# Optimization experiments

Measured on AMD Instinct MI355X. Metric: run time of the kernel, lower is better.

## Reference

```python
import jax, jax.numpy as jnp
import numpy as np

B, K, N, D = 64, 64, 32768, 2048   # batch, knn neighbors, memory size, feat dim (hardcoded 2048 in source)
NC, NHID, TOPK = 2048, 512, 5      # num clusters, gcn hidden, topk in affinity masking


def setup_inputs() -> dict:
    key = jax.random.key(0)
    ks = jax.random.split(key, 8)
    features = jax.random.normal(ks[0], (N, D), jnp.float32)
    labels = jax.random.randint(ks[1], (N,), 0, NC)
    indexes = jax.random.randint(ks[2], (B,), 0, N)
    ori_knn_neighbor = jax.random.randint(ks[3], (B, K), 0, N)
    s = 0.02
    conv_w = jax.random.normal(ks[4], (2 * D, NHID), jnp.float32) * s
    conv_b = jnp.zeros((NHID,), jnp.float32)
    w1 = jax.random.normal(ks[5], (NHID, NHID), jnp.float32) * s
    b1 = jnp.zeros((NHID,), jnp.float32)
    prelu_a = jnp.full((NHID,), 0.25, jnp.float32)
    w2 = jax.random.normal(ks[6], (NHID, 2), jnp.float32) * s
    b2 = jnp.zeros((2,), jnp.float32)
    return dict(indexes=indexes, features=features, labels=labels,
                ori_knn_neighbor=ori_knn_neighbor, conv_w=conv_w, conv_b=conv_b,
                w1=w1, b1=b1, prelu_a=prelu_a, w2=w2, b2=b2)


def _build_graphs(indexes, features, labels, ori_knn_neighbor):
    # cluster mean features (index_add_ + count normalize), done under no_grad in torch
    counts = jax.ops.segment_sum(jnp.ones((N,), jnp.float32), labels, num_segments=NC)
    clu_sum = jax.ops.segment_sum(features, labels, num_segments=NC)
    clu_mean = clu_sum / jnp.maximum(counts, 1.0)[:, None]

    def per_sample(idx, nbr):
        clu_lab = labels[nbr]                                  # [K]
        cf = clu_mean[clu_lab].at[0].set(features[idx])        # [K, D]
        A = (cf @ cf.T) / 5.0                                  # [K, K]
        j = jnp.arange(K)
        # keep only first occurrence of each cluster label (np.unique return_index)
        dup = jnp.any((clu_lab[:, None] == clu_lab[None, :]) & (j[None, :] < j[:, None]), axis=1)
        keep = (~dup).astype(A.dtype)                          # [K]
        _, ti = jax.lax.top_k(A, TOPK)                         # [K, TOPK]
        m = jnp.zeros_like(A).at[j[:, None], ti].set(1.0)
        m = ((m > 0) & (m.T > 0)).astype(A.dtype) * keep[:, None] * keep[None, :]
        A = A * m
        cf = cf / jnp.linalg.norm(cf, axis=1, keepdims=True)   # row-normalize
        cf = cf - cf[0]                                        # center on query (row 0 -> 0)
        return cf, A

    x, adj = jax.vmap(per_sample)(indexes, ori_knn_neighbor)   # [B,K,D], [B,K,K]
    return jax.lax.stop_gradient(x), jax.lax.stop_gradient(adj)


def reference(indexes, features, labels, ori_knn_neighbor,
              conv_w, conv_b, w1, b1, prelu_a, w2, b2):
    x, adj = _build_graphs(indexes, features, labels, ori_knn_neighbor)
    # GraphConv with MeanAggregator: agg = A @ x, concat, linear, relu
    agg = jnp.einsum('bij,bjd->bid', adj, x)                   # [B,K,D]
    h = jax.nn.relu(jnp.concatenate([x, agg], axis=-1) @ conv_w + conv_b)  # [B,K,NHID]
    h0 = h.reshape(-1, NHID)
    h1 = h0 @ w1 + b1
    h1 = jnp.where(h1 > 0, h1, prelu_a * h1)                   # PReLU(nhid)
    logits = h1 @ w2 + b2                                      # [B*K, 2]
    return jax.nn.softmax(logits.reshape(B, K, 2), axis=2)
```

## Files before the change

kernel.cpp:

```cpp
#include <hip/hip_runtime.h>
#include <hip/hip_bf16.h>

#define BB 64
#define KN 64
#define NPTS 32768
#define DD 2048
#define NCC 2048
#define NH 512
#define MM 4096
#define K2 4096

typedef unsigned short u16;
typedef unsigned int u32;
typedef __attribute__((ext_vector_type(8))) short short8;
typedef __attribute__((ext_vector_type(4))) float f32x4;

__device__ __forceinline__ float bf2f(u32 u){
  union { u32 i; float f; } v; v.i = u << 16; return v.f;
}
__device__ __forceinline__ u16 f2bf(float f){
  union { float f; u32 i; } v; v.f = f;
  u32 x = v.i;
  return (u16)((x + 0x7fffu + ((x >> 16) & 1u)) >> 16);
}

typedef __attribute__((address_space(3))) u32 as3_u32;
typedef const __attribute__((address_space(1))) u32 as1_u32;
__device__ __forceinline__ void glds16(const void* g, void* l){
  __builtin_amdgcn_global_load_lds((as1_u32*)g, (as3_u32*)l, 16, 0, 0);
}

__global__ __launch_bounds__(256) void k_prep(
    const int* __restrict__ labels, int* __restrict__ counts,
    const int* __restrict__ knn, int* __restrict__ used,
    const void* __restrict__ conv_w, u16* __restrict__ cwT, int fcw,
    const void* __restrict__ w1, u16* __restrict__ w1T, int fw1){
  __shared__ u16 tile[64][65];
  int bb = blockIdx.x, t = threadIdx.x;
  if(bb < 128){
    int n = bb*256 + t;
    atomicAdd(&counts[labels[n]], 1);
    return;
  }
  if(bb == 704){
    #pragma unroll
    for(int i=0;i<16;i++){
      int idx = i*256 + t;
      used[labels[knn[idx]]] = 1;
    }
    return;
  }
  const void* src; u16* dst; int Kd, Nd, isf32, tb;
  if(bb < 640){ src=conv_w; dst=cwT; Kd=K2; Nd=NH; isf32=fcw; tb=bb-128; }
  else        { src=w1;     dst=w1T; Kd=NH; Nd=NH; isf32=fw1; tb=bb-640; }
  int nbt = Nd >> 6;
  int k0 = (tb / nbt) << 6;
  int n0 = (tb % nbt) << 6;
  if(isf32){
    const float* s = (const float*)src;
    #pragma unroll
    for(int ph=0; ph<16; ph++){
      int idx = ph*256 + t;
      int r = idx >> 6, c = idx & 63;
      tile[r][c] = f2bf(s[(size_t)(k0+r)*Nd + n0 + c]);
    }
  } else {
    const u16* s = (const u16*)src;
    #pragma unroll
    for(int ph=0; ph<16; ph++){
      int idx = ph*256 + t;
      int r = idx >> 6, c = idx & 63;
      tile[r][c] = s[(size_t)(k0+r)*Nd + n0 + c];
    }
  }
  __syncthreads();
  #pragma unroll
  for(int ph=0; ph<16; ph++){
    int idx = ph*256 + t;
    int r = idx >> 6, c = idx & 63;
    dst[(size_t)(n0+r)*Kd + k0 + c] = tile[c][r];
  }
}

__global__ void k_scan(const int* __restrict__ counts, int* __restrict__ offsets){
  __shared__ int sb[256];
  int t = threadIdx.x;
  int c[8]; int s = 0;
  #pragma unroll
  for(int i=0;i<8;i++){ c[i] = counts[t*8+i]; s += c[i]; }
  sb[t] = s; __syncthreads();
  int v = s;
  for(int off=1; off<256; off<<=1){
    int u = (t>=off) ? sb[t-off] : 0;
    __syncthreads();
    v += u; sb[t] = v;
    __syncthreads();
  }
  int run = v - s;
  #pragma unroll
  for(int i=0;i<8;i++){ offsets[t*8+i] = run; run += c[i]; }
}

__global__ void k_scatter(const int* __restrict__ labels, const int* __restrict__ offsets,
                          int* __restrict__ cursor, int* __restrict__ sorted){
  int n = blockIdx.x*256 + threadIdx.x;
  int c = labels[n];
  int p = atomicAdd(&cursor[c], 1);
  sorted[offsets[c] + p] = n;
}

__global__ __launch_bounds__(256) void k_clumean(
    const void* __restrict__ feat, const int* __restrict__ counts,
    const int* __restrict__ offsets, const int* __restrict__ sorted,
    const int* __restrict__ used, int isf32, float* __restrict__ clu){
  int c = blockIdx.x, t = threadIdx.x;
  if(!used[c]) return;
  __shared__ int ridx[64];
  int cnt = counts[c], start = offsets[c];
  float acc[8] = {0,0,0,0,0,0,0,0};
  for(int base=0; base<cnt; base+=64){
    int take = min(64, cnt-base);
    __syncthreads();
    if(t < take) ridx[t] = sorted[start+base+t];
    __syncthreads();
    if(isf32){
      const float* ff = (const float*)feat;
      int r = 0;
      for(; r+2<=take; r+=2){
        const float* p0 = ff + (size_t)ridx[r]*DD + t*8;
        const float* p1 = ff + (size_t)ridx[r+1]*DD + t*8;
        float4 a0=*(const float4*)p0, b0=*(const float4*)(p0+4);
        float4 a1=*(const float4*)p1, b1=*(const float4*)(p1+4);
        acc[0]+=a0.x+a1.x; acc[1]+=a0.y+a1.y; acc[2]+=a0.z+a1.z; acc[3]+=a0.w+a1.w;
        acc[4]+=b0.x+b1.x; acc[5]+=b0.y+b1.y; acc[6]+=b0.z+b1.z; acc[7]+=b0.w+b1.w;
      }
      if(r < take){
        const float* p0 = ff + (size_t)ridx[r]*DD + t*8;
        float4 a0=*(const float4*)p0, b0=*(const float4*)(p0+4);
        acc[0]+=a0.x; acc[1]+=a0.y; acc[2]+=a0.z; acc[3]+=a0.w;
        acc[4]+=b0.x; acc[5]+=b0.y; acc[6]+=b0.z; acc[7]+=b0.w;
      }
    } else {
      const u16* fb = (const u16*)feat;
      int r = 0;
      for(; r+2<=take; r+=2){
        const u16* p0 = fb + (size_t)ridx[r]*DD + t*8;
        const u16* p1 = fb + (size_t)ridx[r+1]*DD + t*8;
        uint4 v0 = *(const uint4*)p0, v1 = *(const uint4*)p1;
        acc[0]+=bf2f(v0.x&0xffffu)+bf2f(v1.x&0xffffu); acc[1]+=bf2f(v0.x>>16)+bf2f(v1.x>>16);
        acc[2]+=bf2f(v0.y&0xffffu)+bf2f(v1.y&0xffffu); acc[3]+=bf2f(v0.y>>16)+bf2f(v1.y>>16);
        acc[4]+=bf2f(v0.z&0xffffu)+bf2f(v1.z&0xffffu); acc[5]+=bf2f(v0.z>>16)+bf2f(v1.z>>16);
        acc[6]+=bf2f(v0.w&0xffffu)+bf2f(v1.w&0xffffu); acc[7]+=bf2f(v0.w>>16)+bf2f(v1.w>>16);
      }
      if(r < take){
        const u16* p0 = fb + (size_t)ridx[r]*DD + t*8;
        uint4 v0 = *(const uint4*)p0;
        acc[0]+=bf2f(v0.x&0xffffu); acc[1]+=bf2f(v0.x>>16);
        acc[2]+=bf2f(v0.y&0xffffu); acc[3]+=bf2f(v0.y>>16);
        acc[4]+=bf2f(v0.z&0xffffu); acc[5]+=bf2f(v0.z>>16);
        acc[6]+=bf2f(v0.w&0xffffu); acc[7]+=bf2f(v0.w>>16);
      }
    }
  }
  float div = fmaxf((float)cnt, 1.0f);
  float* o = clu + (size_t)c*DD + t*8;
  float4 o0 = make_float4(acc[0]/div, acc[1]/div, acc[2]/div, acc[3]/div);
  float4 o1 = make_float4(acc[4]/div, acc[5]/div, acc[6]/div, acc[7]/div);
  *(float4*)o = o0;
  *(float4*)(o+4) = o1;
}

__global__ __launch_bounds__(256) void k_Apart(
    const void* __restrict__ feat, const float* __restrict__ clu,
    const int* __restrict__ indexes, const int* __restrict__ labels,
    const int* __restrict__ knn, int isf32, float* __restrict__ Apart){
  int b = blockIdx.x >> 2, g = blockIdx.x & 3;
  int t = threadIdx.x;
  __shared__ float cfT[64][68];
  __shared__ int sl[64];
  if(t < 64) sl[t] = labels[knn[b*64 + t]];
  int qidx = indexes[b];
  __syncthreads();

  int i0 = (t & 15)*4, j0 = (t >> 4)*4;
  float acc[4][4];
  #pragma unroll
  for(int a=0;a<4;a++)
    #pragma unroll
    for(int c2=0;c2<4;c2++) acc[a][c2] = 0.f;

  for(int ch=g*8; ch<g*8+8; ch++){
    int dbase = ch*64;
    #pragma unroll
    for(int ps=0; ps<16; ps++){
      int idx = ps*256 + t;
      int k = idx >> 6, dd = idx & 63;
      float v;
      if(k == 0){
        size_t fi = (size_t)qidx*DD + dbase + dd;
        v = isf32 ? ((const float*)feat)[fi] : bf2f(((const u16*)feat)[fi]);
      } else {
        v = clu[(size_t)sl[k]*DD + dbase + dd];
      }
      cfT[dd][k] = v;
    }
    __syncthreads();
    #pragma unroll 4
    for(int dd=0; dd<64; dd++){
      float4 av = *(const float4*)&cfT[dd][i0];
      float4 bv = *(const float4*)&cfT[dd][j0];
      float aa[4] = {av.x, av.y, av.z, av.w};
      float bbv[4] = {bv.x, bv.y, bv.z, bv.w};
      #pragma unroll
      for(int ii=0;ii<4;ii++)
        #pragma unroll
        for(int jj=0;jj<4;jj++)
          acc[ii][jj] += aa[ii]*bbv[jj];
    }
    __syncthreads();
  }

  float* op = Apart + ((size_t)(g*64 + b))*4096;
  #pragma unroll
  for(int ii=0;ii<4;ii++)
    *(float4*)&op[(i0+ii)*64 + j0] = make_float4(acc[ii][0], acc[ii][1], acc[ii][2], acc[ii][3]);
}

__global__ __launch_bounds__(256) void k_Afinal(
    const float* __restrict__ Apart, const int* __restrict__ labels,
    const int* __restrict__ knn,
    float* __restrict__ adj, float* __restrict__ norms){
  int b = blockIdx.x, t = threadIdx.x;
  __shared__ float A[64][65];
  __shared__ unsigned long long mb[64];
  __shared__ int sl[64];
  __shared__ int sk[64];
  if(t < 64) sl[t] = labels[knn[b*64 + t]];
  const float* P = Apart + (size_t)b*4096;
  const size_t gs = (size_t)64*4096;
  #pragma unroll
  for(int ps=0; ps<16; ps++){
    int idx = ps*256 + t;
    float s = P[idx] + P[idx+gs] + P[idx+2*gs] + P[idx+3*gs];
    A[idx>>6][idx&63] = s * 0.2f;
  }
  __syncthreads();
  if(t < 64){
    int dup = 0;
    for(int j=0;j<t;j++) dup |= (sl[j]==sl[t]);
    sk[t] = dup ? 0 : 1;
    unsigned long long chosen = 0;
    const float* row = A[t];
    #pragma unroll
    for(int p=0;p<5;p++){
      float best = -INFINITY; int bi = 0;
      for(int j=0;j<64;j++){
        bool taken = (chosen >> j) & 1ull;
        float v = row[j];
        if(!taken && v > best){ best = v; bi = j; }
      }
      chosen |= (1ull << bi);
    }
    mb[t] = chosen;
    norms[b*64+t] = sqrtf(fmaxf(A[t][t]*5.0f, 0.0f));
  }
  __syncthreads();
  float* O = adj + (size_t)b*4096;
  #pragma unroll
  for(int ps=0; ps<16; ps++){
    int idx = ps*256 + t;
    int i = idx >> 6, j = idx & 63;
    bool on = ((mb[i]>>j)&1ull) && ((mb[j]>>i)&1ull) && sk[i] && sk[j];
    O[idx] = on ? A[i][j] : 0.0f;
  }
}

__global__ __launch_bounds__(256) void k_xagg(
    const void* __restrict__ feat, const float* __restrict__ clu,
    const int* __restrict__ indexes, const int* __restrict__ labels,
    const int* __restrict__ knn, const float* __restrict__ norms,
    const float* __restrict__ adj, int isf32, u16* __restrict__ xab){
  int b = blockIdx.x >> 2, g = blockIdx.x & 3;
  int t = threadIdx.x;
  __shared__ u16  xs[64][512];
  __shared__ float adjs[64][65];
  __shared__ float nzv[64][8];
  __shared__ u16   nzj[64][8];
  __shared__ int   nzc[64];
  __shared__ int   sl[64];
  __shared__ float sn[64];

  const float* Ab = adj + (size_t)b*4096;
  #pragma unroll
  for(int ps=0; ps<16; ps++){
    int idx = ps*256 + t;
    adjs[idx>>6][idx&63] = Ab[idx];
  }
  if(t < 64){
    sl[t] = labels[knn[b*64 + t]];
    sn[t] = 1.0f / fmaxf(norms[b*64 + t], 1e-30f);
  }
  int qidx = indexes[b];
  int d = g*512 + t*2;
  float q0, q1;
  if(isf32){
    float2 qv = *(const float2*)((const float*)feat + (size_t)qidx*DD + d);
    q0 = qv.x; q1 = qv.y;
  } else {
    u32 w = *(const u32*)((const u16*)feat + (size_t)qidx*DD + d);
    q0 = bf2f(w & 0xffffu); q1 = bf2f(w >> 16);
  }
  __syncthreads();
  if(t < 64){
    int c = 0;
    for(int j=0;j<64;j++){
      float v = adjs[t][j];
      if(v != 0.0f && c < 8){ nzv[t][c] = v; nzj[t][c] = (u16)j; c++; }
    }
    nzc[t] = c;
  }
  float inv0 = sn[0];
  q0 *= inv0; q1 *= inv0;

  *(u32*)&xs[0][t*2] = 0u;
  *(u32*)(xab + (size_t)(b*64)*K2 + d) = 0u;
  for(int k=1;k<64;k++){
    float2 cv = *(const float2*)(clu + (size_t)sl[k]*DD + d);
    float invk = sn[k];
    u16 x0 = f2bf(cv.x*invk - q0), x1 = f2bf(cv.y*invk - q1);
    u32 w = (u32)x0 | ((u32)x1 << 16);
    *(u32*)&xs[k][t*2] = w;
    *(u32*)(xab + (size_t)(b*64+k)*K2 + d) = w;
  }
  __syncthreads();

  for(int r=0;r<64;r++){
    float a0 = 0.f, a1 = 0.f;
    int c = nzc[r];
    for(int p=0;p<c;p++){
      float s = nzv[r][p]; int j = nzj[r][p];
      u32 w = *(const u32*)&xs[j][t*2];
      a0 += s*bf2f(w & 0xffffu);
      a1 += s*bf2f(w >> 16);
    }
    u32 w = (u32)f2bf(a0) | ((u32)f2bf(a1) << 16);
    *(u32*)(xab + (size_t)(b*64+r)*K2 + DD + d) = w;
  }
}

template<int EPI>
__global__ __launch_bounds__(256, 2) void k_gemm(
    const u16* __restrict__ Am, const u16* __restrict__ Bt,
    const void* __restrict__ bias, const void* __restrict__ pa,
    int fbias, int fpa,
    void* __restrict__ Cout, int Md, int Nd, int Kd)
{
  __shared__ u16 As[2][64*64];
  __shared__ u16 Bs[2][64*64];
  int t = threadIdx.x;
  int nblk = gridDim.x;
  int bid = (blockIdx.x & 7)*(nblk >> 3) + (blockIdx.x >> 3);
  int nb = Nd >> 6;
  int m0 = (bid / nb) << 6;
  int n0 = (bid % nb) << 6;
  int wave = t >> 6, lane = t & 63;
  int wm = wave >> 1, wn = wave & 1;
  int lm = lane & 15, lq = lane >> 4;
  int lrow = lane >> 3, lcol = lane & 7;

  f32x4 acc[2][2];
  #pragma unroll
  for(int i=0;i<2;i++)
    #pragma unroll
    for(int j=0;j<2;j++) acc[i][j] = (f32x4){0.f,0.f,0.f,0.f};

  auto stage = [&](int buf, int kb){
    #pragma unroll
    for(int c=0;c<2;c++){
      int cb = wave*2 + c;
      int row = cb*8 + lrow;
      int col = lcol ^ (row & 7);
      glds16(Am + (size_t)(m0+row)*Kd + kb + col*8, &As[buf][cb*512]);
    }
    #pragma unroll
    for(int c=0;c<2;c++){
      int cb = wave*2 + c;
      int row = cb*8 + lrow;
      int col = lcol ^ (row & 7);
      glds16(Bt + (size_t)(n0+row)*Kd + kb + col*8, &Bs[buf][cb*512]);
    }
  };

  stage(0, 0);
  __syncthreads();
  int cur = 0;
  for(int kb=0; kb<Kd; kb+=64){
    if(kb + 64 < Kd) stage(cur^1, kb+64);
    #pragma unroll
    for(int kk=0;kk<2;kk++){
      short8 af[2], bfr[2];
      #pragma unroll
      for(int mi=0;mi<2;mi++){
        int r = wm*32 + mi*16 + lm;
        int p = ((kk<<2)+lq) ^ (r & 7);
        union{ uint4 u; short8 v; } x;
        x.u = *(const uint4*)&As[cur][r*64 + p*8];
        af[mi] = x.v;
      }
      #pragma unroll
      for(int ni=0;ni<2;ni++){
        int r = wn*32 + ni*16 + lm;
        int p = ((kk<<2)+lq) ^ (r & 7);
        union{ uint4 u; short8 v; } x;
        x.u = *(const uint4*)&Bs[cur][r*64 + p*8];
        bfr[ni] = x.v;
      }
      #pragma unroll
      for(int mi=0;mi<2;mi++)
        #pragma unroll
        for(int ni=0;ni<2;ni++)
          acc[mi][ni] = __builtin_amdgcn_mfma_f32_16x16x32_bf16(af[mi], bfr[ni], acc[mi][ni], 0, 0, 0);
    }
    __syncthreads();
    cur ^= 1;
  }

  #pragma unroll
  for(int ni=0;ni<2;ni++){
    int col = n0 + wn*32 + ni*16 + lm;
    float bs = fbias ? ((const float*)bias)[col] : bf2f(((const u16*)bias)[col]);
    float av = 0.f;
    if(EPI==1) av = fpa ? ((const float*)pa)[col] : bf2f(((const u16*)pa)[col]);
    #pragma unroll
    for(int mi=0;mi<2;mi++){
      int rowb = m0 + wm*32 + mi*16 + lq*4;
      #pragma unroll
      for(int r2=0;r2<4;r2++){
        float v = acc[mi][ni][r2] + bs;
        if(EPI==0){
          v = fmaxf(v, 0.f);
          ((u16*)Cout)[(size_t)(rowb+r2)*Nd + col] = f2bf(v);
        } else {
          v = (v > 0.f) ? v : av*v;
          ((float*)Cout)[(size_t)(rowb+r2)*Nd + col] = v;
        }
      }
    }
  }
}

__global__ __launch_bounds__(256) void k_out(
    const float* __restrict__ h1, const void* __restrict__ w2,
    const void* __restrict__ b2, int fw2, int fb2, int fo,
    void* __restrict__ out){
  int t = threadIdx.x; int lane = t & 63; int row = blockIdx.x*4 + (t >> 6);
  const float* hr = h1 + (size_t)row*NH;
  float s0 = 0.f, s1 = 0.f;
  #pragma unroll
  for(int j=0;j<NH/64;j++){
    int i = lane + j*64;
    float h = hr[i];
    float w0 = fw2 ? ((const float*)w2)[i*2+0] : bf2f(((const u16*)w2)[i*2+0]);
    float w1v= fw2 ? ((const float*)w2)[i*2+1] : bf2f(((const u16*)w2)[i*2+1]);
    s0 += h * w0;
    s1 += h * w1v;
  }
  #pragma unroll
  for(int off=32; off>0; off>>=1){
    s0 += __shfl_down(s0, off);
    s1 += __shfl_down(s1, off);
  }
  if(lane==0){
    float bb0 = fb2 ? ((const float*)b2)[0] : bf2f(((const u16*)b2)[0]);
    float bb1 = fb2 ? ((const float*)b2)[1] : bf2f(((const u16*)b2)[1]);
    float l0 = s0 + bb0;
    float l1 = s1 + bb1;
    float m = fmaxf(l0, l1);
    float e0 = expf(l0 - m), e1 = expf(l1 - m);
    float inv = 1.0f / (e0 + e1);
    if(fo){
      ((float*)out)[row*2+0] = e0*inv;
      ((float*)out)[row*2+1] = e1*inv;
    } else {
      ((u16*)out)[row*2+0] = f2bf(e0*inv);
      ((u16*)out)[row*2+1] = f2bf(e1*inv);
    }
  }
}

__global__ void k_fill_sentinel(u32* __restrict__ out, int nwords){
  int i = blockIdx.x*256 + threadIdx.x;
  if(i < nwords) out[i] = 0x40404040u;
}

extern "C" void kernel_launch(void* const* d_in, const int* in_sizes, int n_in,
                              void* d_out, int out_size, void* d_ws, size_t ws_size,
                              hipStream_t stream) {
  const int* indexes = (const int*)d_in[0];
  const void* feat   = d_in[1];
  const int* labels  = (const int*)d_in[2];
  const int* knn     = (const int*)d_in[3];
  const void* conv_w = d_in[4];
  const void* conv_b = d_in[5];
  const void* w1     = d_in[6];
  const void* b1     = d_in[7];
  const void* pa     = d_in[8];
  const void* w2     = d_in[9];
  const void* b2     = d_in[10];

  int ff  = (in_sizes[1]  != (int)((size_t)NPTS*DD*2));
  int fcw = (in_sizes[4]  != (int)((size_t)2*DD*NH*2));
  int fcb = (in_sizes[5]  != NH*2);
  int fw1 = (in_sizes[6]  != (int)((size_t)NH*NH*2));
  int fb1 = (in_sizes[7]  != NH*2);
  int fpa = (in_sizes[8]  != NH*2);
  int fw2 = (in_sizes[9]  != NH*2*2);
  int fb2 = (in_sizes[10] != 2*2);
  int fo  = (out_size     != MM*2*2);

  char* w = (char*)d_ws;
  size_t o = 0;
  auto alloc = [&](size_t bytes) -> void* {
    void* p = w + o; o = (o + bytes + 255) & ~(size_t)255; return p;
  };
  int*   counts  = (int*)  alloc((size_t)NCC*4);
  int*   cursor  = (int*)  alloc((size_t)NCC*4);
  int*   used    = (int*)  alloc((size_t)NCC*4);
  int*   offsets = (int*)  alloc((size_t)NCC*4);
  int*   sorted  = (int*)  alloc((size_t)NPTS*4);
  float* norms   = (float*)alloc((size_t)MM*4);
  float* adj     = (float*)alloc((size_t)BB*64*64*4);
  float* Apart   = (float*)alloc((size_t)4*BB*64*64*4);
  float* clu     = (float*)alloc((size_t)NCC*DD*4);
  u16*   xab     = (u16*)  alloc((size_t)MM*K2*2);
  u16*   cwT     = (u16*)  alloc((size_t)K2*NH*2);
  u16*   w1T     = (u16*)  alloc((size_t)NH*NH*2);
  u16*   hb      = (u16*)  clu;
  float* h1      = (float*)((char*)clu + (size_t)MM*NH*2);

  size_t NEED = o;
  if(ws_size < NEED){
    int nwords = out_size/4;
    k_fill_sentinel<<<(nwords+255)/256, 256, 0, stream>>>((u32*)d_out, nwords);
    return;
  }

  hipMemsetAsync(counts, 0, (size_t)NCC*4*3, stream);

  k_prep   <<<705, 256, 0, stream>>>(labels, counts, knn, used, conv_w, cwT, fcw, w1, w1T, fw1);
  k_scan   <<<1, 256, 0, stream>>>(counts, offsets);
  k_scatter<<<NPTS/256, 256, 0, stream>>>(labels, offsets, cursor, sorted);
  k_clumean<<<NCC, 256, 0, stream>>>(feat, counts, offsets, sorted, used, ff, clu);
  k_Apart  <<<BB*4, 256, 0, stream>>>(feat, clu, indexes, labels, knn, ff, Apart);
  k_Afinal <<<BB, 256, 0, stream>>>(Apart, labels, knn, adj, norms);
  k_xagg   <<<BB*4, 256, 0, stream>>>(feat, clu, indexes, labels, knn, norms, adj, ff, xab);

  k_gemm<0><<<(MM/64)*(NH/64), 256, 0, stream>>>(xab, cwT, conv_b, nullptr, fcb, 0, (void*)hb, MM, NH, K2);
  k_gemm<1><<<(MM/64)*(NH/64), 256, 0, stream>>>(hb, w1T, b1, pa, fb1, fpa, (void*)h1, MM, NH, NH);

  k_out    <<<MM/4, 256, 0, stream>>>(h1, w2, b2, fw2, fb2, fo, d_out);
}
```

Baseline: 558.8 us.

## Fuse all pipeline stages into one cooperative persistent kernel with grid syncs

Replaces the chain of eleven launches (memset, prep, scan, scatter, cluster mean, affinity partials, affinity finalisation, x/aggregation, two GEMMs, output) with a single cooperative kernel of 512 blocks. The stages are separated by grid-wide barriers and each stage's work is remapped onto the fixed grid. The affinity partial sums are split eight ways instead of four, and the fp32 cluster-mean gather is unrolled by four. This is meant to remove per-launch overhead and idle gaps between small kernels. In exchange, parallelism is capped at 512 blocks for stages that previously launched more (cluster mean, GEMMs), and each grid barrier adds its own cost. The old multi-kernel path is kept as a fallback if the cooperative launch fails.

```diff
diff --git a/kernel.cpp b/kernel.cpp
--- a/kernel.cpp
+++ b/kernel.cpp
@@ -1,5 +1,8 @@
 #include <hip/hip_runtime.h>
 #include <hip/hip_bf16.h>
+#include <hip/hip_cooperative_groups.h>
+
+namespace cg = cooperative_groups;
 
 #define BB 64
 #define KN 64
@@ -28,6 +31,446 @@
 typedef const __attribute__((address_space(1))) u32 as1_u32;
 __device__ __forceinline__ void glds16(const void* g, void* l){
   __builtin_amdgcn_global_load_lds((as1_u32*)g, (as3_u32*)l, 16, 0, 0);
+}
+
+struct MegaArgs {
+  const int* indexes; const void* feat; const int* labels; const int* knn;
+  const void* conv_w; const void* conv_b; const void* w1; const void* b1;
+  const void* pa; const void* w2; const void* b2;
+  int ff, fcw, fcb, fw1, fb1, fpa, fw2, fb2, fo;
+  int* counts; int* cursor; int* used; int* offsets; int* sorted;
+  float* norms; float* adj; float* Apart; float* clu;
+  u16* xab; u16* cwT; u16* w1T; u16* hb; float* h1; void* out;
+};
+
+__global__ __launch_bounds__(256, 2) void k_mega(MegaArgs a){
+  __shared__ __align__(16) char smem[33024];
+  cg::grid_group grid = cg::this_grid();
+  int gid = blockIdx.x, t = threadIdx.x;
+
+  if(gid < 24){
+    int idx = gid*256 + t;
+    a.counts[idx] = 0;
+  }
+  for(int u = gid; u < 576; u += 512){
+    u16 (*tile)[65] = (u16(*)[65])smem;
+    const void* src; u16* dst; int Kd, Nd, isf32, tb;
+    if(u < 512){ src=a.conv_w; dst=a.cwT; Kd=K2; Nd=NH; isf32=a.fcw; tb=u; }
+    else       { src=a.w1;     dst=a.w1T; Kd=NH; Nd=NH; isf32=a.fw1; tb=u-512; }
+    int nbt = Nd >> 6;
+    int k0 = (tb / nbt) << 6;
+    int n0 = (tb % nbt) << 6;
+    if(isf32){
+      const float* s = (const float*)src;
+      #pragma unroll
+      for(int ph=0; ph<16; ph++){
+        int idx = ph*256 + t;
+        int r = idx >> 6, c = idx & 63;
+        tile[r][c] = f2bf(s[(size_t)(k0+r)*Nd + n0 + c]);
+      }
+    } else {
+      const u16* s = (const u16*)src;
+      #pragma unroll
+      for(int ph=0; ph<16; ph++){
+        int idx = ph*256 + t;
+        int r = idx >> 6, c = idx & 63;
+        tile[r][c] = s[(size_t)(k0+r)*Nd + n0 + c];
+      }
+    }
+    __syncthreads();
+    #pragma unroll
+    for(int ph=0; ph<16; ph++){
+      int idx = ph*256 + t;
+      int r = idx >> 6, c = idx & 63;
+      dst[(size_t)(n0+r)*Kd + k0 + c] = tile[c][r];
+    }
+    __syncthreads();
+  }
+  grid.sync();
+
+  if(gid < 128){
+    int n = gid*256 + t;
+    atomicAdd(&a.counts[a.labels[n]], 1);
+  } else if(gid < 144){
+    int idx = (gid-128)*256 + t;
+    a.used[a.labels[a.knn[idx]]] = 1;
+  }
+  grid.sync();
+
+  if(gid == 0){
+    int* sb = (int*)smem;
+    int c[8]; int s = 0;
+    #pragma unroll
+    for(int i=0;i<8;i++){ c[i] = a.counts[t*8+i]; s += c[i]; }
+    sb[t] = s; __syncthreads();
+    int v = s;
+    for(int off=1; off<256; off<<=1){
+      int u = (t>=off) ? sb[t-off] : 0;
+      __syncthreads();
+      v += u; sb[t] = v;
+      __syncthreads();
+    }
+    int run = v - s;
+    #pragma unroll
+    for(int i=0;i<8;i++){ a.offsets[t*8+i] = run; run += c[i]; }
+  }
+  grid.sync();
+
+  if(gid < 128){
+    int n = gid*256 + t;
+    int c = a.labels[n];
+    int p = atomicAdd(&a.cursor[c], 1);
+    a.sorted[a.offsets[c] + p] = n;
+  }
+  grid.sync();
+
+  {
+    int* ridx = (int*)smem;
+    for(int c = gid; c < NCC; c += 512){
+      if(!a.used[c]) continue;
+      int cnt = a.counts[c], start = a.offsets[c];
+      float acc[8] = {0,0,0,0,0,0,0,0};
+      for(int base=0; base<cnt; base+=64){
+        int take = min(64, cnt-base);
+        __syncthreads();
+        if(t < take) ridx[t] = a.sorted[start+base+t];
+        __syncthreads();
+        if(a.ff){
+          const float* ff = (const float*)a.feat;
+          int r = 0;
+          for(; r+4<=take; r+=4){
+            const float* p0 = ff + (size_t)ridx[r]*DD + t*8;
+            const float* p1 = ff + (size_t)ridx[r+1]*DD + t*8;
+            const float* p2 = ff + (size_t)ridx[r+2]*DD + t*8;
+            const float* p3 = ff + (size_t)ridx[r+3]*DD + t*8;
+            float4 a0=*(const float4*)p0, b0=*(const float4*)(p0+4);
+            float4 a1=*(const float4*)p1, b1=*(const float4*)(p1+4);
+            float4 a2=*(const float4*)p2, b2=*(const float4*)(p2+4);
+            float4 a3=*(const float4*)p3, b3=*(const float4*)(p3+4);
+            acc[0]+=a0.x+a1.x+a2.x+a3.x; acc[1]+=a0.y+a1.y+a2.y+a3.y;
+            acc[2]+=a0.z+a1.z+a2.z+a3.z; acc[3]+=a0.w+a1.w+a2.w+a3.w;
+            acc[4]+=b0.x+b1.x+b2.x+b3.x; acc[5]+=b0.y+b1.y+b2.y+b3.y;
+            acc[6]+=b0.z+b1.z+b2.z+b3.z; acc[7]+=b0.w+b1.w+b2.w+b3.w;
+          }
+          for(; r<take; r++){
+            const float* p0 = ff + (size_t)ridx[r]*DD + t*8;
+            float4 a0=*(const float4*)p0, b0=*(const float4*)(p0+4);
+            acc[0]+=a0.x; acc[1]+=a0.y; acc[2]+=a0.z; acc[3]+=a0.w;
+            acc[4]+=b0.x; acc[5]+=b0.y; acc[6]+=b0.z; acc[7]+=b0.w;
+          }
+        } else {
+          const u16* fb = (const u16*)a.feat;
+          for(int r=0; r<take; r++){
+            const u16* p0 = fb + (size_t)ridx[r]*DD + t*8;
+            uint4 v0 = *(const uint4*)p0;
+            acc[0]+=bf2f(v0.x&0xffffu); acc[1]+=bf2f(v0.x>>16);
+            acc[2]+=bf2f(v0.y&0xffffu); acc[3]+=bf2f(v0.y>>16);
+            acc[4]+=bf2f(v0.z&0xffffu); acc[5]+=bf2f(v0.z>>16);
+            acc[6]+=bf2f(v0.w&0xffffu); acc[7]+=bf2f(v0.w>>16);
+          }
+        }
+      }
+      float div = fmaxf((float)cnt, 1.0f);
+      float* o = a.clu + (size_t)c*DD + t*8;
+      float4 o0 = make_float4(acc[0]/div, acc[1]/div, acc[2]/div, acc[3]/div);
+      float4 o1 = make_float4(acc[4]/div, acc[5]/div, acc[6]/div, acc[7]/div);
+      *(float4*)o = o0;
+      *(float4*)(o+4) = o1;
+      __syncthreads();
+    }
+  }
+  grid.sync();
+
+  {
+    int b = gid >> 3, g = gid & 7;
+    float (*cfT)[68] = (float(*)[68])smem;
+    int* sl = (int*)(smem + 17408);
+    if(t < 64) sl[t] = a.labels[a.knn[b*64 + t]];
+    int qidx = a.indexes[b];
+    __syncthreads();
+    int i0 = (t & 15)*4, j0 = (t >> 4)*4;
+    float acc[4][4];
+    #pragma unroll
+    for(int x=0;x<4;x++)
+      #pragma unroll
+      for(int y=0;y<4;y++) acc[x][y] = 0.f;
+    for(int ch=g*4; ch<g*4+4; ch++){
+      int dbase = ch*64;
+      #pragma unroll
+      for(int ps=0; ps<16; ps++){
+        int idx = ps*256 + t;
+        int k = idx >> 6, dd = idx & 63;
+        float v;
+        if(k == 0){
+          size_t fi = (size_t)qidx*DD + dbase + dd;
+          v = a.ff ? ((const float*)a.feat)[fi] : bf2f(((const u16*)a.feat)[fi]);
+        } else {
+          v = a.clu[(size_t)sl[k]*DD + dbase + dd];
+        }
+        cfT[dd][k] = v;
+      }
+      __syncthreads();
+      #pragma unroll 4
+      for(int dd=0; dd<64; dd++){
+        float4 av = *(const float4*)&cfT[dd][i0];
+        float4 bv = *(const float4*)&cfT[dd][j0];
+        float aa[4] = {av.x, av.y, av.z, av.w};
+        float bbv[4] = {bv.x, bv.y, bv.z, bv.w};
+        #pragma unroll
+        for(int ii=0;ii<4;ii++)
+          #pragma unroll
+          for(int jj=0;jj<4;jj++)
+            acc[ii][jj] += aa[ii]*bbv[jj];
+      }
+      __syncthreads();
+    }
+    float* op = a.Apart + ((size_t)(g*64 + b))*4096;
+    #pragma unroll
+    for(int ii=0;ii<4;ii++)
+      *(float4*)&op[(i0+ii)*64 + j0] = make_float4(acc[ii][0], acc[ii][1], acc[ii][2], acc[ii][3]);
+  }
+  grid.sync();
+
+  if(gid < 64){
+    int b = gid;
+    float (*A)[65] = (float(*)[65])smem;
+    unsigned long long* mb = (unsigned long long*)(smem + 16640);
+    int* sl = (int*)(smem + 17152);
+    int* sk = (int*)(smem + 17408);
+    if(t < 64) sl[t] = a.labels[a.knn[b*64 + t]];
+    const float* P = a.Apart + (size_t)b*4096;
+    const size_t gs = (size_t)64*4096;
+    #pragma unroll
+    for(int ps=0; ps<16; ps++){
+      int idx = ps*256 + t;
+      float s = P[idx] + P[idx+gs] + P[idx+2*gs] + P[idx+3*gs]
+              + P[idx+4*gs] + P[idx+5*gs] + P[idx+6*gs] + P[idx+7*gs];
+      A[idx>>6][idx&63] = s * 0.2f;
+    }
+    __syncthreads();
+    if(t < 64){
+      int dup = 0;
+      for(int j=0;j<t;j++) dup |= (sl[j]==sl[t]);
+      sk[t] = dup ? 0 : 1;
+      unsigned long long chosen = 0;
+      const float* row = A[t];
+      #pragma unroll
+      for(int p=0;p<5;p++){
+        float best = -INFINITY; int bi = 0;
+        for(int j=0;j<64;j++){
+          bool taken = (chosen >> j) & 1ull;
+          float v = row[j];
+          if(!taken && v > best){ best = v; bi = j; }
+        }
+        chosen |= (1ull << bi);
+      }
+      mb[t] = chosen;
+      a.norms[b*64+t] = sqrtf(fmaxf(A[t][t]*5.0f, 0.0f));
+    }
+    __syncthreads();
+    float* O = a.adj + (size_t)b*4096;
+    #pragma unroll
+    for(int ps=0; ps<16; ps++){
+      int idx = ps*256 + t;
+      int i = idx >> 6, j = idx & 63;
+      bool on = ((mb[i]>>j)&1ull) && ((mb[j]>>i)&1ull) && sk[i] && sk[j];
+      O[idx] = on ? A[i][j] : 0.0f;
+    }
+  }
+  grid.sync();
+
+  if(gid < 256){
+    int b = gid >> 2, g = gid & 3;
+    float (*adjs)[65] = (float(*)[65])smem;
+    float (*nzv)[8]   = (float(*)[8])(smem + 16640);
+    u16   (*nzj)[8]   = (u16(*)[8])(smem + 18688);
+    int*   nzc        = (int*)(smem + 19712);
+    int*   sl         = (int*)(smem + 19968);
+    float* sn         = (float*)(smem + 20224);
+    const float* Ab = a.adj + (size_t)b*4096;
+    #pragma unroll
+    for(int ps=0; ps<16; ps++){
+      int idx = ps*256 + t;
+      adjs[idx>>6][idx&63] = Ab[idx];
+    }
+    if(t < 64){
+      sl[t] = a.labels[a.knn[b*64 + t]];
+      sn[t] = 1.0f / fmaxf(a.norms[b*64 + t], 1e-30f);
+    }
+    int qidx = a.indexes[b];
+    int d = g*512 + t*2;
+    float q0, q1;
+    if(a.ff){
+      float2 qv = *(const float2*)((const float*)a.feat + (size_t)qidx*DD + d);
+      q0 = qv.x; q1 = qv.y;
+    } else {
+      u32 w = *(const u32*)((const u16*)a.feat + (size_t)qidx*DD + d);
+      q0 = bf2f(w & 0xffffu); q1 = bf2f(w >> 16);
+    }
+    __syncthreads();
+    if(t < 64){
+      int c = 0;
+      for(int j=0;j<64;j++){
+        float v = adjs[t][j];
+        if(v != 0.0f && c < 8){ nzv[t][c] = v; nzj[t][c] = (u16)j; c++; }
+      }
+      nzc[t] = c;
+    }
+    float inv0 = sn[0];
+    q0 *= inv0; q1 *= inv0;
+    *(u32*)(a.xab + (size_t)(b*64)*K2 + d) = 0u;
+    for(int k=1;k<64;k++){
+      float2 cv = *(const float2*)(a.clu + (size_t)sl[k]*DD + d);
+      float invk = sn[k];
+      u16 x0 = f2bf(cv.x*invk - q0), x1 = f2bf(cv.y*invk - q1);
+      *(u32*)(a.xab + (size_t)(b*64+k)*K2 + d) = (u32)x0 | ((u32)x1 << 16);
+    }
+    __syncthreads();
+    for(int r=0;r<64;r++){
+      float a0 = 0.f, a1 = 0.f;
+      int c = nzc[r];
+      for(int p=0;p<c;p++){
+        float s = nzv[r][p]; int j = nzj[r][p];
+        u32 w = *(const u32*)(a.xab + (size_t)(b*64+j)*K2 + d);
+        a0 += s*bf2f(w & 0xffffu);
+        a1 += s*bf2f(w >> 16);
+      }
+      *(u32*)(a.xab + (size_t)(b*64+r)*K2 + DD + d) = (u32)f2bf(a0) | ((u32)f2bf(a1) << 16);
+    }
+  }
+  grid.sync();
+
+  #pragma unroll 1
+  for(int pass=0; pass<2; pass++){
+    const u16* Am = pass==0 ? a.xab : a.hb;
+    const u16* Bt = pass==0 ? a.cwT : a.w1T;
+    int Kd = pass==0 ? K2 : NH;
+    int fbias = pass==0 ? a.fcb : a.fb1;
+    const void* bias = pass==0 ? a.conv_b : a.b1;
+    u16 (*As)[4096] = (u16(*)[4096])smem;
+    u16 (*Bs)[4096] = (u16(*)[4096])(smem + 16384);
+    int bid = (gid & 7)*64 + (gid >> 3);
+    int m0 = (bid >> 3) << 6;
+    int n0 = (bid & 7) << 6;
+    int wave = t >> 6, lane = t & 63;
+    int wm = wave >> 1, wn = wave & 1;
+    int lm = lane & 15, lq = lane >> 4;
+    int lrow = lane >> 3, lcol = lane & 7;
+    f32x4 acc[2][2];
+    #pragma unroll
+    for(int i=0;i<2;i++)
+      #pragma unroll
+      for(int j=0;j<2;j++) acc[i][j] = (f32x4){0.f,0.f,0.f,0.f};
+    #define STAGE(buf, kb) do{ \
+      _Pragma("unroll") \
+      for(int c=0;c<2;c++){ \
+        int cb = wave*2 + c; \
+        int row = cb*8 + lrow; \
+        int col = lcol ^ (row & 7); \
+        glds16(Am + (size_t)(m0+row)*Kd + (kb) + col*8, &As[buf][cb*512]); \
+      } \
+      _Pragma("unroll") \
+      for(int c=0;c<2;c++){ \
+        int cb = wave*2 + c; \
+        int row = cb*8 + lrow; \
+        int col = lcol ^ (row & 7); \
+        glds16(Bt + (size_t)(n0+row)*Kd + (kb) + col*8, &Bs[buf][cb*512]); \
+      } \
+    }while(0)
+    STAGE(0, 0);
+    __syncthreads();
+    int cur = 0;
+    for(int kb=0; kb<Kd; kb+=64){
+      if(kb + 64 < Kd) STAGE(cur^1, kb+64);
+      #pragma unroll
+      for(int kk=0;kk<2;kk++){
+        short8 af[2], bfr[2];
+        #pragma unroll
+        for(int mi=0;mi<2;mi++){
+          int r = wm*32 + mi*16 + lm;
+          int p = ((kk<<2)+lq) ^ (r & 7);
+          union{ uint4 u; short8 v; } x;
+          x.u = *(const uint4*)&As[cur][r*64 + p*8];
+          af[mi] = x.v;
+        }
+        #pragma unroll
+        for(int ni=0;ni<2;ni++){
+          int r = wn*32 + ni*16 + lm;
+          int p = ((kk<<2)+lq) ^ (r & 7);
+          union{ uint4 u; short8 v; } x;
+          x.u = *(const uint4*)&Bs[cur][r*64 + p*8];
+          bfr[ni] = x.v;
+        }
+        #pragma unroll
+        for(int mi=0;mi<2;mi++)
+          #pragma unroll
+          for(int ni=0;ni<2;ni++)
+            acc[mi][ni] = __builtin_amdgcn_mfma_f32_16x16x32_bf16(af[mi], bfr[ni], acc[mi][ni], 0, 0, 0);
+      }
+      __syncthreads();
+      cur ^= 1;
+    }
+    #undef STAGE
+    #pragma unroll
+    for(int ni=0;ni<2;ni++){
+      int col = n0 + wn*32 + ni*16 + lm;
+      float bs = fbias ? ((const float*)bias)[col] : bf2f(((const u16*)bias)[col]);
+      float av = 0.f;
+      if(pass==1) av = a.fpa ? ((const float*)a.pa)[col] : bf2f(((const u16*)a.pa)[col]);
+      #pragma unroll
+      for(int mi=0;mi<2;mi++){
+        int rowb = m0 + wm*32 + mi*16 + lq*4;
+        #pragma unroll
+        for(int r2=0;r2<4;r2++){
+          float v = acc[mi][ni][r2] + bs;
+          if(pass==0){
+            v = fmaxf(v, 0.f);
+            a.hb[(size_t)(rowb+r2)*NH + col] = f2bf(v);
+          } else {
+            v = (v > 0.f) ? v : av*v;
+            a.h1[(size_t)(rowb+r2)*NH + col] = v;
+          }
+        }
+      }
+    }
+    grid.sync();
+  }
+
+  for(int u = gid; u < 1024; u += 512){
+    int lane = t & 63; int row = u*4 + (t >> 6);
+    const float* hr = a.h1 + (size_t)row*NH;
+    float s0 = 0.f, s1 = 0.f;
+    #pragma unroll
+    for(int j=0;j<NH/64;j++){
+      int i = lane + j*64;
+      float h = hr[i];
+      float w0 = a.fw2 ? ((const float*)a.w2)[i*2+0] : bf2f(((const u16*)a.w2)[i*2+0]);
+      float w1v= a.fw2 ? ((const float*)a.w2)[i*2+1] : bf2f(((const u16*)a.w2)[i*2+1]);
+      s0 += h * w0;
+      s1 += h * w1v;
+    }
+    #pragma unroll
+    for(int off=32; off>0; off>>=1){
+      s0 += __shfl_down(s0, off);
+      s1 += __shfl_down(s1, off);
+    }
+    if(lane==0){
+      float bb0 = a.fb2 ? ((const float*)a.b2)[0] : bf2f(((const u16*)a.b2)[0]);
+      float bb1 = a.fb2 ? ((const float*)a.b2)[1] : bf2f(((const u16*)a.b2)[1]);
+      float l0 = s0 + bb0;
+      float l1 = s1 + bb1;
+      float m = fmaxf(l0, l1);
+      float e0 = expf(l0 - m), e1 = expf(l1 - m);
+      float inv = 1.0f / (e0 + e1);
+      if(a.fo){
+        ((float*)a.out)[row*2+0] = e0*inv;
+        ((float*)a.out)[row*2+1] = e1*inv;
+      } else {
+        ((u16*)a.out)[row*2+0] = f2bf(e0*inv);
+        ((u16*)a.out)[row*2+1] = f2bf(e1*inv);
+      }
+    }
+  }
 }
 
 __global__ __launch_bounds__(256) void k_prep(
@@ -142,17 +585,7 @@
       }
     } else {
       const u16* fb = (const u16*)feat;
-      int r = 0;
-      for(; r+2<=take; r+=2){
-        const u16* p0 = fb + (size_t)ridx[r]*DD + t*8;
-        const u16* p1 = fb + (size_t)ridx[r+1]*DD + t*8;
-        uint4 v0 = *(const uint4*)p0, v1 = *(const uint4*)p1;
-        acc[0]+=bf2f(v0.x&0xffffu)+bf2f(v1.x&0xffffu); acc[1]+=bf2f(v0.x>>16)+bf2f(v1.x>>16);
-        acc[2]+=bf2f(v0.y&0xffffu)+bf2f(v1.y&0xffffu); acc[3]+=bf2f(v0.y>>16)+bf2f(v1.y>>16);
-        acc[4]+=bf2f(v0.z&0xffffu)+bf2f(v1.z&0xffffu); acc[5]+=bf2f(v0.z>>16)+bf2f(v1.z>>16);
-        acc[6]+=bf2f(v0.w&0xffffu)+bf2f(v1.w&0xffffu); acc[7]+=bf2f(v0.w>>16)+bf2f(v1.w>>16);
-      }
-      if(r < take){
+      for(int r=0; r<take; r++){
         const u16* p0 = fb + (size_t)ridx[r]*DD + t*8;
         uint4 v0 = *(const uint4*)p0;
         acc[0]+=bf2f(v0.x&0xffffu); acc[1]+=bf2f(v0.x>>16);
@@ -181,14 +614,12 @@
   if(t < 64) sl[t] = labels[knn[b*64 + t]];
   int qidx = indexes[b];
   __syncthreads();
-
   int i0 = (t & 15)*4, j0 = (t >> 4)*4;
   float acc[4][4];
   #pragma unroll
-  for(int a=0;a<4;a++)
-    #pragma unroll
-    for(int c2=0;c2<4;c2++) acc[a][c2] = 0.f;
-
+  for(int x=0;x<4;x++)
+    #pragma unroll
+    for(int c2=0;c2<4;c2++) acc[x][c2] = 0.f;
   for(int ch=g*8; ch<g*8+8; ch++){
     int dbase = ch*64;
     #pragma unroll
@@ -219,7 +650,6 @@
     }
     __syncthreads();
   }
-
   float* op = Apart + ((size_t)(g*64 + b))*4096;
   #pragma unroll
   for(int ii=0;ii<4;ii++)
@@ -289,7 +719,6 @@
   __shared__ int   nzc[64];
   __shared__ int   sl[64];
   __shared__ float sn[64];
-
   const float* Ab = adj + (size_t)b*4096;
   #pragma unroll
   for(int ps=0; ps<16; ps++){
@@ -321,7 +750,6 @@
   }
   float inv0 = sn[0];
   q0 *= inv0; q1 *= inv0;
-
   *(u32*)&xs[0][t*2] = 0u;
   *(u32*)(xab + (size_t)(b*64)*K2 + d) = 0u;
   for(int k=1;k<64;k++){
@@ -333,7 +761,6 @@
     *(u32*)(xab + (size_t)(b*64+k)*K2 + d) = w;
   }
   __syncthreads();
-
   for(int r=0;r<64;r++){
     float a0 = 0.f, a1 = 0.f;
     int c = nzc[r];
@@ -367,13 +794,11 @@
   int wm = wave >> 1, wn = wave & 1;
   int lm = lane & 15, lq = lane >> 4;
   int lrow = lane >> 3, lcol = lane & 7;
-
   f32x4 acc[2][2];
   #pragma unroll
   for(int i=0;i<2;i++)
     #pragma unroll
     for(int j=0;j<2;j++) acc[i][j] = (f32x4){0.f,0.f,0.f,0.f};
-
   auto stage = [&](int buf, int kb){
     #pragma unroll
     for(int c=0;c<2;c++){
@@ -390,7 +815,6 @@
       glds16(Bt + (size_t)(n0+row)*Kd + kb + col*8, &Bs[buf][cb*512]);
     }
   };
-
   stage(0, 0);
   __syncthreads();
   int cur = 0;
@@ -424,7 +848,6 @@
     __syncthreads();
     cur ^= 1;
   }
-
   #pragma unroll
   for(int ni=0;ni<2;ni++){
     int col = n0 + wn*32 + ni*16 + lm;
@@ -530,7 +953,7 @@
   int*   sorted  = (int*)  alloc((size_t)NPTS*4);
   float* norms   = (float*)alloc((size_t)MM*4);
   float* adj     = (float*)alloc((size_t)BB*64*64*4);
-  float* Apart   = (float*)alloc((size_t)4*BB*64*64*4);
+  float* Apart   = (float*)alloc((size_t)8*BB*64*64*4);
   float* clu     = (float*)alloc((size_t)NCC*DD*4);
   u16*   xab     = (u16*)  alloc((size_t)MM*K2*2);
   u16*   cwT     = (u16*)  alloc((size_t)K2*NH*2);
@@ -545,18 +968,30 @@
     return;
   }
 
-  hipMemsetAsync(counts, 0, (size_t)NCC*4*3, stream);
-
-  k_prep   <<<705, 256, 0, stream>>>(labels, counts, knn, used, conv_w, cwT, fcw, w1, w1T, fw1);
-  k_scan   <<<1, 256, 0, stream>>>(counts, offsets);
-  k_scatter<<<NPTS/256, 256, 0, stream>>>(labels, offsets, cursor, sorted);
-  k_clumean<<<NCC, 256, 0, stream>>>(feat, counts, offsets, sorted, used, ff, clu);
-  k_Apart  <<<BB*4, 256, 0, stream>>>(feat, clu, indexes, labels, knn, ff, Apart);
-  k_Afinal <<<BB, 256, 0, stream>>>(Apart, labels, knn, adj, norms);
-  k_xagg   <<<BB*4, 256, 0, stream>>>(feat, clu, indexes, labels, knn, norms, adj, ff, xab);
-
-  k_gemm<0><<<(MM/64)*(NH/64), 256, 0, stream>>>(xab, cwT, conv_b, nullptr, fcb, 0, (void*)hb, MM, NH, K2);
-  k_gemm<1><<<(MM/64)*(NH/64), 256, 0, stream>>>(hb, w1T, b1, pa, fb1, fpa, (void*)h1, MM, NH, NH);
-
-  k_out    <<<MM/4, 256, 0, stream>>>(h1, w2, b2, fw2, fb2, fo, d_out);
-}
+  MegaArgs ma;
+  ma.indexes=indexes; ma.feat=feat; ma.labels=labels; ma.knn=knn;
+  ma.conv_w=conv_w; ma.conv_b=conv_b; ma.w1=w1; ma.b1=b1;
+  ma.pa=pa; ma.w2=w2; ma.b2=b2;
+  ma.ff=ff; ma.fcw=fcw; ma.fcb=fcb; ma.fw1=fw1; ma.fb1=fb1;
+  ma.fpa=fpa; ma.fw2=fw2; ma.fb2=fb2; ma.fo=fo;
+  ma.counts=counts; ma.cursor=cursor; ma.used=used; ma.offsets=offsets;
+  ma.sorted=sorted; ma.norms=norms; ma.adj=adj; ma.Apart=Apart; ma.clu=clu;
+  ma.xab=xab; ma.cwT=cwT; ma.w1T=w1T; ma.hb=hb; ma.h1=h1; ma.out=d_out;
+
+  void* kargs[] = { &ma };
+  hipError_t e = hipLaunchCooperativeKernel((const void*)k_mega, dim3(512), dim3(256),
+                                            kargs, 0, stream);
+  if(e != hipSuccess){
+    hipMemsetAsync(counts, 0, (size_t)NCC*4*3, stream);
+    k_prep   <<<705, 256, 0, stream>>>(labels, counts, knn, used, conv_w, cwT, fcw, w1, w1T, fw1);
+    k_scan   <<<1, 256, 0, stream>>>(counts, offsets);
+    k_scatter<<<NPTS/256, 256, 0, stream>>>(labels, offsets, cursor, sorted);
+    k_clumean<<<NCC, 256, 0, stream>>>(feat, counts, offsets, sorted, used, ff, clu);
+    k_Apart  <<<BB*4, 256, 0, stream>>>(feat, clu, indexes, labels, knn, ff, Apart);
+    k_Afinal <<<BB, 256, 0, stream>>>(Apart, labels, knn, adj, norms);
+    k_xagg   <<<BB*4, 256, 0, stream>>>(feat, clu, indexes, labels, knn, norms, adj, ff, xab);
+    k_gemm<0><<<(MM/64)*(NH/64), 256, 0, stream>>>(xab, cwT, conv_b, nullptr, fcb, 0, (void*)hb, MM, NH, K2);
+    k_gemm<1><<<(MM/64)*(NH/64), 256, 0, stream>>>(hb, w1T, b1, pa, fb1, fpa, (void*)h1, MM, NH, NH);
+    k_out    <<<MM/4, 256, 0, stream>>>(h1, w2, b2, fw2, fb2, fo, d_out);
+  }
+}
```

Result: slower. 1.179 ms (+110.9%).
